# Kernel tuning notes

Hardware: AMD Instinct MI355X
Metric: run time of the kernel (lower is better)

The kernel has to match this reference:

```python
import jax, jax.numpy as jnp
import numpy as np

N_NODES = 100000
IN_DIM, HID_DIM, OUT_DIM = 1433, 16, 7
N_EDGES = 3200000


def gcn_conv(x, edge_index, W, b, num_nodes):
    # add self loops
    loop = jnp.arange(num_nodes, dtype=edge_index.dtype)
    src = jnp.concatenate([edge_index[0], loop])  # [E+N]
    dst = jnp.concatenate([edge_index[1], loop])
    h = x @ W + b  # [N, out]
    # degree computed on row (edge_index[0]) as in the torch code
    deg = jax.ops.segment_sum(jnp.ones_like(src, dtype=h.dtype), src,
                              num_segments=num_nodes)
    dis = deg ** -0.5  # self-loops guarantee deg >= 1
    norm = dis[src] * dis[dst]  # [E+N]
    msg = norm[:, None] * h[src]  # gather + scale
    return jax.ops.segment_sum(msg, dst, num_segments=num_nodes)  # scatter-add


def setup_inputs() -> dict:
    key = jax.random.key(0)
    k1, k2, k3, k4, k5, k6 = jax.random.split(key, 6)
    x = jax.random.normal(k1, (N_NODES, IN_DIM), dtype=jnp.float32)
    edge_index = jax.random.randint(k2, (2, N_EDGES), 0, N_NODES, dtype=jnp.int64)
    s1 = 1.0 / np.sqrt(IN_DIM)
    s2 = 1.0 / np.sqrt(HID_DIM)
    W1 = jax.random.uniform(k3, (IN_DIM, HID_DIM), jnp.float32, -s1, s1)
    b1 = jax.random.uniform(k4, (HID_DIM,), jnp.float32, -s1, s1)
    W2 = jax.random.uniform(k5, (HID_DIM, OUT_DIM), jnp.float32, -s2, s2)
    b2 = jax.random.uniform(k6, (OUT_DIM,), jnp.float32, -s2, s2)
    return {"x": x, "edge_index": edge_index, "W1": W1, "b1": b1,
            "W2": W2, "b2": b2}


def reference(x, edge_index, W1, b1, W2, b2):
    n = x.shape[0]
    h = gcn_conv(x, edge_index, W1, b1, n)
    h = jax.nn.relu(h)
    # dropout is inactive in eval mode (training=False)
    h = gcn_conv(h, edge_index, W2, b2, n)
    return jax.nn.log_softmax(h, axis=1)
```

## Files before the change

kernel.cpp:

```cpp
#include <hip/hip_runtime.h>
#include <math.h>

constexpr int IN_DIM = 1433;
constexpr int HID    = 16;
constexpr int OUTD   = 7;

__device__ __forceinline__ int edge_get(const int* __restrict__ ei, long long idx, int is64) {
    return is64 ? ei[2 * idx] : ei[idx];
}

__global__ void k_detect(const int* __restrict__ ei, int* __restrict__ flag) {
    __shared__ int nzsh;
    if (threadIdx.x == 0) nzsh = 0;
    __syncthreads();
    int nz = 0;
    for (int i = threadIdx.x; i < 2048; i += blockDim.x)
        nz |= (ei[2 * i + 1] != 0) ? 1 : 0;
    if (nz) nzsh = 1;
    __syncthreads();
    if (threadIdx.x == 0) *flag = (nzsh == 0) ? 1 : 0;
}

__global__ void k_init_new(int* __restrict__ deg, int* __restrict__ cnt, int n) {
    int i = blockIdx.x * blockDim.x + threadIdx.x;
    if (i < n) { deg[i] = 1; cnt[i] = 0; }
}

__global__ void k_deg_finish(float* __restrict__ dis, int n) {
    int i = blockIdx.x * blockDim.x + threadIdx.x;
    if (i < n) {
        int v = ((const int*)dis)[i];
        dis[i] = rsqrtf((float)v);
    }
}

__global__ __launch_bounds__(128) void k_gemm1h(
        const float* __restrict__ x, const float* __restrict__ W1,
        const float* __restrict__ b1, float* __restrict__ h1, int n,
        const int* __restrict__ ei, int E, const int* __restrict__ flag,
        int* __restrict__ deg, int* __restrict__ cnt, int nHist) {
    if ((int)blockIdx.x < nHist) {
        int is64 = *flag;
        long long stride = (long long)nHist * blockDim.x;
        for (long long e = (long long)blockIdx.x * blockDim.x + threadIdx.x;
             e < E; e += stride) {
            int s = edge_get(ei, e, is64);
            int d = edge_get(ei, (long long)E + e, is64);
            atomicAdd(&deg[s], 1);
            atomicAdd(&cnt[d], 1);
        }
        return;
    }

    constexpr int BK = 32, XST = 36;
    __shared__ __align__(16) float xs[128 * XST];
    __shared__ __align__(16) float wsm[BK * HID];
    const int t    = threadIdx.x;
    const int c4   = t & 3;
    const int rq   = t >> 2;
    const int row0 = ((int)blockIdx.x - nHist) * 128;

    float xreg[32];
    float wreg[4];
    float acc[16];
    #pragma unroll
    for (int j = 0; j < 16; ++j) acc[j] = 0.f;

    auto issue = [&](int kt) {
        #pragma unroll
        for (int i = 0; i < 32; ++i) {
            int idx  = t + 128 * i;
            int srow = idx >> 5;
            int scol = idx & 31;
            int gr   = row0 + srow;
            int col  = kt + scol;
            float v = 0.f;
            if (gr < n && col < IN_DIM) v = x[(long long)gr * IN_DIM + col];
            xreg[i] = v;
        }
        #pragma unroll
        for (int u = 0; u < 4; ++u) {
            int idx = t + 128 * u;
            int kk  = idx >> 4;
            wreg[u] = (kt + kk < IN_DIM) ? W1[(kt + kk) * HID + (idx & 15)] : 0.f;
        }
    };
    auto commit = [&]() {
        #pragma unroll
        for (int i = 0; i < 32; ++i) {
            int idx  = t + 128 * i;
            int srow = idx >> 5;
            int scol = idx & 31;
            xs[srow * XST + scol] = xreg[i];
        }
        #pragma unroll
        for (int u = 0; u < 4; ++u) wsm[t + 128 * u] = wreg[u];
    };

    const int nkt = (IN_DIM + BK - 1) / BK;
    issue(0);
    for (int it = 0; it < nkt; ++it) {
        commit();
        __syncthreads();
        if (it + 1 < nkt) issue((it + 1) * BK);
        #pragma unroll 8
        for (int k = 0; k < BK; ++k) {
            float4 w = *(const float4*)&wsm[k * HID + c4 * 4];
            #pragma unroll
            for (int j = 0; j < 4; ++j) {
                float xv = xs[(rq + 32 * j) * XST + k];
                acc[j * 4 + 0] += xv * w.x;
                acc[j * 4 + 1] += xv * w.y;
                acc[j * 4 + 2] += xv * w.z;
                acc[j * 4 + 3] += xv * w.w;
            }
        }
        __syncthreads();
    }

    float4 bv = *(const float4*)&b1[c4 * 4];
    #pragma unroll
    for (int j = 0; j < 4; ++j) {
        int gr = row0 + rq + 32 * j;
        if (gr < n) {
            float4 hv;
            hv.x = acc[j * 4 + 0] + bv.x;
            hv.y = acc[j * 4 + 1] + bv.y;
            hv.z = acc[j * 4 + 2] + bv.z;
            hv.w = acc[j * 4 + 3] + bv.w;
            *(float4*)&h1[(long long)gr * HID + c4 * 4] = hv;
        }
    }
}

__global__ void k_scale(const float* __restrict__ dis, const float* __restrict__ in,
                        float* __restrict__ out, int n, int squared) {
    int i = blockIdx.x * blockDim.x + threadIdx.x;
    if (i >= n * 4) return;
    int row = i >> 2;
    float d = dis[row];
    if (squared) d *= d;
    float4 v = *(const float4*)&in[(long long)i * 4];
    v.x *= d; v.y *= d; v.z *= d; v.w *= d;
    *(float4*)&out[(long long)i * 4] = v;
}

__global__ __launch_bounds__(256) void k_scan1(const int* __restrict__ cnt,
                                               int* __restrict__ bsum, int n) {
    __shared__ int sh[256];
    int t = threadIdx.x;
    int base = blockIdx.x * 1024 + t * 4;
    int s = 0;
    #pragma unroll
    for (int j = 0; j < 4; ++j) {
        int i = base + j;
        if (i < n) s += cnt[i];
    }
    sh[t] = s; __syncthreads();
    for (int o = 128; o > 0; o >>= 1) {
        if (t < o) sh[t] += sh[t + o];
        __syncthreads();
    }
    if (t == 0) bsum[blockIdx.x] = sh[0];
}

__global__ __launch_bounds__(256) void k_scan2(const int* __restrict__ bsum,
                                               int* __restrict__ boff,
                                               int* __restrict__ rp,
                                               int nb, int n, int E) {
    __shared__ int sh[256];
    int t = threadIdx.x;
    int v = (t < nb) ? bsum[t] : 0;
    sh[t] = v; __syncthreads();
    for (int o = 1; o < 256; o <<= 1) {
        int tmp = (t >= o) ? sh[t - o] : 0;
        __syncthreads();
        sh[t] += tmp;
        __syncthreads();
    }
    boff[t] = sh[t] - v;
    if (t == 0) rp[n] = E;
}

__global__ __launch_bounds__(256) void k_scan3(const int* __restrict__ cnt,
                                               const int* __restrict__ boff,
                                               int* __restrict__ rp,
                                               int* __restrict__ cur, int n) {
    __shared__ int sh[256];
    int t = threadIdx.x;
    int base = blockIdx.x * 1024 + t * 4;
    int c[4];
    int s = 0;
    #pragma unroll
    for (int j = 0; j < 4; ++j) {
        int i = base + j;
        c[j] = (i < n) ? cnt[i] : 0;
        s += c[j];
    }
    sh[t] = s; __syncthreads();
    for (int o = 1; o < 256; o <<= 1) {
        int tmp = (t >= o) ? sh[t - o] : 0;
        __syncthreads();
        sh[t] += tmp;
        __syncthreads();
    }
    int run = boff[blockIdx.x] + sh[t] - s;
    #pragma unroll
    for (int j = 0; j < 4; ++j) {
        int i = base + j;
        if (i < n) { rp[i] = run; cur[i] = run; }
        run += c[j];
    }
}

__global__ void k_fill(const int* __restrict__ ei, int E, const int* __restrict__ flag,
                       int* __restrict__ cur, int* __restrict__ csr) {
    int e = blockIdx.x * blockDim.x + threadIdx.x;
    if (e >= E) return;
    int is64 = *flag;
    int s = edge_get(ei, e, is64);
    int d = edge_get(ei, (long long)E + e, is64);
    int slot = atomicAdd(&cur[d], 1);
    csr[slot] = s;
}

__global__ __launch_bounds__(256) void k_gather1f(
        const int* __restrict__ rp, const int* __restrict__ csr,
        const float* __restrict__ dis, const float* __restrict__ hs1,
        const float* __restrict__ W2, const float* __restrict__ b2,
        float* __restrict__ hs2, int n) {
    __shared__ float w2s[HID * OUTD];
    __shared__ float b2s[OUTD];
    int t = threadIdx.x;
    if (t < HID * OUTD) w2s[t] = W2[t];
    if (t < OUTD) b2s[t] = b2[t];
    __syncthreads();

    int tid  = blockIdx.x * blockDim.x + t;
    int node = tid >> 2;
    int q    = tid & 3;
    if (node >= n) return;

    float4 acc = *(const float4*)&hs1[(long long)node * HID + q * 4];

    int i = rp[node], end = rp[node + 1];
    if (i < end) {
        int    s1  = csr[i];
        float4 hv1 = *(const float4*)&hs1[(long long)s1 * HID + q * 4];
        for (++i; i < end; ++i) {
            int    s2  = csr[i];
            float4 hv2 = *(const float4*)&hs1[(long long)s2 * HID + q * 4];
            acc.x += hv1.x; acc.y += hv1.y; acc.z += hv1.z; acc.w += hv1.w;
            hv1 = hv2;
        }
        acc.x += hv1.x; acc.y += hv1.y; acc.z += hv1.z; acc.w += hv1.w;
    }

    float dn = dis[node];
    float r0 = fmaxf(dn * acc.x, 0.f), r1 = fmaxf(dn * acc.y, 0.f);
    float r2 = fmaxf(dn * acc.z, 0.f), r3 = fmaxf(dn * acc.w, 0.f);
    float p[OUTD];
    #pragma unroll
    for (int j = 0; j < OUTD; ++j) {
        p[j] = r0 * w2s[(q * 4 + 0) * OUTD + j]
             + r1 * w2s[(q * 4 + 1) * OUTD + j]
             + r2 * w2s[(q * 4 + 2) * OUTD + j]
             + r3 * w2s[(q * 4 + 3) * OUTD + j];
    }
    #pragma unroll
    for (int j = 0; j < OUTD; ++j) {
        p[j] += __shfl_xor(p[j], 1, 4);
        p[j] += __shfl_xor(p[j], 2, 4);
    }
    hs2[(long long)node * OUTD + q] = dn * (p[q] + b2s[q]);
    if (q < 3) hs2[(long long)node * OUTD + q + 4] = dn * (p[q + 4] + b2s[q + 4]);
}

__global__ __launch_bounds__(256) void k_gather2(
        const int* __restrict__ rp, const int* __restrict__ csr,
        const float* __restrict__ dis, const float* __restrict__ hs2,
        float* __restrict__ out, int n) {
    int t = threadIdx.x;
    int node = blockIdx.x * 32 + (t >> 3);
    int q = t & 7;
    if (node >= n) return;
    float acc = -1e30f;
    if (q < OUTD) {
        acc = hs2[(long long)node * OUTD + q];
        int i = rp[node], end = rp[node + 1];
        if (i < end) {
            int   s1 = csr[i];
            float v1 = hs2[(long long)s1 * OUTD + q];
            for (++i; i < end; ++i) {
                int   s2 = csr[i];
                float v2 = hs2[(long long)s2 * OUTD + q];
                acc += v1;
                v1 = v2;
            }
            acc += v1;
        }
        acc *= dis[node];
    }
    float m = acc;
    #pragma unroll
    for (int o = 1; o < 8; o <<= 1) m = fmaxf(m, __shfl_xor(m, o, 8));
    float ex = (q < OUTD) ? expf(acc - m) : 0.f;
    float ss = ex;
    #pragma unroll
    for (int o = 1; o < 8; o <<= 1) ss += __shfl_xor(ss, o, 8);
    if (q < OUTD) out[(long long)node * OUTD + q] = acc - m - logf(ss);
}

__global__ void k_deg_init(int* __restrict__ deg, int n) {
    int i = blockIdx.x * blockDim.x + threadIdx.x;
    if (i < n) deg[i] = 1;
}

__global__ void k_deg_count(const int* __restrict__ ei, int E,
                            const int* __restrict__ flag, int* __restrict__ deg) {
    int e = blockIdx.x * blockDim.x + threadIdx.x;
    if (e >= E) return;
    int is64 = *flag;
    int s = edge_get(ei, e, is64);
    atomicAdd(&deg[s], 1);
}

__global__ void k_agg1(const int* __restrict__ ei, int E, const int* __restrict__ flag,
                       const float* __restrict__ dis, const float* __restrict__ h1,
                       float* __restrict__ a1) {
    long long tid = (long long)blockIdx.x * blockDim.x + threadIdx.x;
    int e = (int)(tid >> 2);
    int q = (int)(tid & 3);
    if (e >= E) return;
    int is64 = *flag;
    int s = edge_get(ei, e, is64);
    int d = edge_get(ei, (long long)E + e, is64);
    float nrm = dis[s] * dis[d];
    float4 v = *(const float4*)&h1[(long long)s * HID + q * 4];
    float* o = &a1[(long long)d * HID + q * 4];
    atomicAdd(o + 0, nrm * v.x);
    atomicAdd(o + 1, nrm * v.y);
    atomicAdd(o + 2, nrm * v.z);
    atomicAdd(o + 3, nrm * v.w);
}

__global__ __launch_bounds__(256) void k_gemm2(
        const float* __restrict__ a1, const float* __restrict__ W2,
        const float* __restrict__ b2, const float* __restrict__ dis,
        float* __restrict__ h2, float* __restrict__ a2, int n) {
    __shared__ float w2s[HID * OUTD];
    __shared__ float b2s[OUTD];
    int t = threadIdx.x;
    if (t < HID * OUTD) w2s[t] = W2[t];
    if (t < OUTD) b2s[t] = b2[t];
    __syncthreads();
    int r = blockIdx.x * blockDim.x + t;
    if (r >= n) return;
    float a[16];
    #pragma unroll
    for (int i = 0; i < 4; ++i) {
        float4 v = *(const float4*)&a1[(long long)r * HID + i * 4];
        a[4 * i + 0] = fmaxf(v.x, 0.f);
        a[4 * i + 1] = fmaxf(v.y, 0.f);
        a[4 * i + 2] = fmaxf(v.z, 0.f);
        a[4 * i + 3] = fmaxf(v.w, 0.f);
    }
    float dd = 0.f;
    if (a2) { float d = dis[r]; dd = d * d; }
    #pragma unroll
    for (int j = 0; j < OUTD; ++j) {
        float acc = b2s[j];
        #pragma unroll
        for (int k = 0; k < HID; ++k) acc += a[k] * w2s[k * OUTD + j];
        h2[(long long)r * OUTD + j] = acc;
        if (a2) a2[(long long)r * OUTD + j] = dd * acc;
    }
}

__global__ void k_agg2(const int* __restrict__ ei, int E, const int* __restrict__ flag,
                       const float* __restrict__ dis, const float* __restrict__ h2,
                       float* __restrict__ a2) {
    long long tid = (long long)blockIdx.x * blockDim.x + threadIdx.x;
    int e = (int)(tid >> 1);
    int q = (int)(tid & 1);
    if (e >= E) return;
    int is64 = *flag;
    int s = edge_get(ei, e, is64);
    int d = edge_get(ei, (long long)E + e, is64);
    float nrm = dis[s] * dis[d];
    int cnt = q ? 3 : 4;
    long long bs = (long long)s * OUTD + q * 4;
    long long bd = (long long)d * OUTD + q * 4;
    #pragma unroll
    for (int j = 0; j < 4; ++j)
        if (j < cnt) atomicAdd(&a2[bd + j], nrm * h2[bs + j]);
}

__global__ void k_lsm(const float* __restrict__ a2, float* __restrict__ out, int n) {
    int r = blockIdx.x * blockDim.x + threadIdx.x;
    if (r >= n) return;
    float v[OUTD];
    #pragma unroll
    for (int j = 0; j < OUTD; ++j) v[j] = a2[(long long)r * OUTD + j];
    float m = v[0];
    #pragma unroll
    for (int j = 1; j < OUTD; ++j) m = fmaxf(m, v[j]);
    float ssum = 0.f;
    #pragma unroll
    for (int j = 0; j < OUTD; ++j) ssum += expf(v[j] - m);
    float l = logf(ssum);
    #pragma unroll
    for (int j = 0; j < OUTD; ++j) out[(long long)r * OUTD + j] = v[j] - m - l;
}

extern "C" void kernel_launch(void* const* d_in, const int* in_sizes, int n_in,
                              void* d_out, int out_size, void* d_ws, size_t ws_size,
                              hipStream_t stream) {
    const float* x  = (const float*)d_in[0];
    const int*   ei = (const int*)d_in[1];
    const float* W1 = (const float*)d_in[2];
    const float* b1 = (const float*)d_in[3];
    const float* W2 = (const float*)d_in[4];
    const float* b2 = (const float*)d_in[5];
    float* out = (float*)d_out;

    const int N = in_sizes[0] / IN_DIM;
    const int E = in_sizes[1] / 2;

    const int TPB = 256;
    const int gN  = (N + TPB - 1) / TPB;
    const int gE  = (E + TPB - 1) / TPB;
    const int gG1 = (N + 127) / 128;
    const int NB  = (N + 1023) / 1024;
    const int nHist = 512;

    float* ws = (float*)d_ws;
    size_t o = 0;
    auto take = [&](size_t cnt) { size_t r = o; o += (cnt + 127) & ~(size_t)127; return r; };

    size_t off_dis  = take((size_t)N);
    size_t off_flag = take(64);
    size_t off_cnt  = take((size_t)N);
    size_t off_rp   = take((size_t)N + 1);
    size_t off_cur  = take((size_t)N);
    size_t off_bs   = take(256);
    size_t off_bo   = take(256);
    size_t off_csr  = take((size_t)E);
    size_t off_h1   = take((size_t)N * HID);
    size_t off_h2   = take((size_t)N * OUTD);
    size_t need_new = o * sizeof(float);

    if (ws_size >= need_new) {
        float* dis  = ws + off_dis;
        int*   degi = (int*)dis;
        int*   flag = (int*)(ws + off_flag);
        int*   cnt  = (int*)(ws + off_cnt);
        int*   rp   = (int*)(ws + off_rp);
        int*   cur  = (int*)(ws + off_cur);
        int*   bs   = (int*)(ws + off_bs);
        int*   bo   = (int*)(ws + off_bo);
        int*   csr  = (int*)(ws + off_csr);
        float* h1   = ws + off_h1;
        float* hs2  = ws + off_h2;

        k_detect<<<1, 256, 0, stream>>>(ei, flag);
        k_init_new<<<gN, TPB, 0, stream>>>(degi, cnt, N);
        k_gemm1h<<<nHist + gG1, 128, 0, stream>>>(x, W1, b1, h1, N,
                                                  ei, E, flag, degi, cnt, nHist);
        k_deg_finish<<<gN, TPB, 0, stream>>>(dis, N);
        k_scan1<<<NB, 256, 0, stream>>>(cnt, bs, N);
        k_scan2<<<1, 256, 0, stream>>>(bs, bo, rp, NB, N, E);
        k_scan3<<<NB, 256, 0, stream>>>(cnt, bo, rp, cur, N);
        k_scale<<<(int)(((long long)N * 4 + TPB - 1) / TPB), TPB, 0, stream>>>(
            dis, h1, h1, N, 0);
        k_fill<<<gE, TPB, 0, stream>>>(ei, E, flag, cur, csr);
        k_gather1f<<<(int)(((long long)N * 4 + TPB - 1) / TPB), TPB, 0, stream>>>(
            rp, csr, dis, h1, W2, b2, hs2, N);
        k_gather2<<<(N + 31) / 32, 256, 0, stream>>>(rp, csr, dis, hs2, out, N);
    } else {
        o = 0;
        size_t f_dis  = take((size_t)N);
        size_t f_flag = take(64);
        size_t f_h1   = take((size_t)N * HID);
        size_t f_a1   = take((size_t)N * HID);
        size_t f_h2   = take((size_t)N * OUTD);
        size_t f_a2   = take((size_t)N * OUTD);

        float* dis  = ws + f_dis;
        int*   degi = (int*)dis;
        int*   flag = (int*)(ws + f_flag);
        float* h1   = ws + f_h1;
        float* a1   = ws + f_a1;
        float* h2   = ws + f_h2;
        float* a2   = ws + f_a2;

        int g4E = (int)(((long long)4 * E + TPB - 1) / TPB);
        int g2E = (int)(((long long)2 * E + TPB - 1) / TPB);

        k_detect<<<1, 256, 0, stream>>>(ei, flag);
        k_deg_init<<<gN, TPB, 0, stream>>>(degi, N);
        k_deg_count<<<gE, TPB, 0, stream>>>(ei, E, flag, degi);
        k_deg_finish<<<gN, TPB, 0, stream>>>(dis, N);
        k_gemm1h<<<gG1, 128, 0, stream>>>(x, W1, b1, h1, N,
                                          ei, E, flag, nullptr, nullptr, 0);
        k_scale<<<(int)(((long long)N * 4 + TPB - 1) / TPB), TPB, 0, stream>>>(
            dis, h1, a1, N, 1);
        k_agg1<<<g4E, TPB, 0, stream>>>(ei, E, flag, dis, h1, a1);
        k_gemm2<<<gN, TPB, 0, stream>>>(a1, W2, b2, dis, h2, a2, N);
        k_agg2<<<g2E, TPB, 0, stream>>>(ei, E, flag, dis, h2, a2);
        k_lsm<<<gN, TPB, 0, stream>>>(a2, out, N);
    }
}
```

Measured before the change: 776.4 us.

## Replace shared-memory tiled first-layer GEMM with direct per-row float4 streaming

The first-layer GEMM no longer stages x and W1 tiles through LDS with register double-buffering. Each thread now streams its own x row with float4 loads, for two rows per thread, and reads W1 directly from global/cache. Block size goes from 128 to 256 threads, which also changes the work split of the fused histogram blocks. The aim is to drop LDS traffic and barriers in this memory-bound pass. The cost is strided, partly misaligned per-row global loads (row stride 1433), which may coalesce worse and lean on L1/L2 reuse.

Result: slower. 985.3 us (+26.9%).

```diff
diff --git a/kernel.cpp b/kernel.cpp
--- a/kernel.cpp
+++ b/kernel.cpp
@@ -34,7 +34,7 @@
     }
 }
 
-__global__ __launch_bounds__(128) void k_gemm1h(
+__global__ __launch_bounds__(256) void k_gemm1h(
         const float* __restrict__ x, const float* __restrict__ W1,
         const float* __restrict__ b1, float* __restrict__ h1, int n,
         const int* __restrict__ ei, int E, const int* __restrict__ flag,
@@ -52,84 +52,56 @@
         return;
     }
 
-    constexpr int BK = 32, XST = 36;
-    __shared__ __align__(16) float xs[128 * XST];
-    __shared__ __align__(16) float wsm[BK * HID];
     const int t    = threadIdx.x;
     const int c4   = t & 3;
-    const int rq   = t >> 2;
+    const int rr   = t >> 2;
     const int row0 = ((int)blockIdx.x - nHist) * 128;
-
-    float xreg[32];
-    float wreg[4];
-    float acc[16];
-    #pragma unroll
-    for (int j = 0; j < 16; ++j) acc[j] = 0.f;
-
-    auto issue = [&](int kt) {
-        #pragma unroll
-        for (int i = 0; i < 32; ++i) {
-            int idx  = t + 128 * i;
-            int srow = idx >> 5;
-            int scol = idx & 31;
-            int gr   = row0 + srow;
-            int col  = kt + scol;
-            float v = 0.f;
-            if (gr < n && col < IN_DIM) v = x[(long long)gr * IN_DIM + col];
-            xreg[i] = v;
-        }
-        #pragma unroll
-        for (int u = 0; u < 4; ++u) {
-            int idx = t + 128 * u;
-            int kk  = idx >> 4;
-            wreg[u] = (kt + kk < IN_DIM) ? W1[(kt + kk) * HID + (idx & 15)] : 0.f;
-        }
-    };
-    auto commit = [&]() {
-        #pragma unroll
-        for (int i = 0; i < 32; ++i) {
-            int idx  = t + 128 * i;
-            int srow = idx >> 5;
-            int scol = idx & 31;
-            xs[srow * XST + scol] = xreg[i];
-        }
-        #pragma unroll
-        for (int u = 0; u < 4; ++u) wsm[t + 128 * u] = wreg[u];
-    };
-
-    const int nkt = (IN_DIM + BK - 1) / BK;
-    issue(0);
-    for (int it = 0; it < nkt; ++it) {
-        commit();
-        __syncthreads();
-        if (it + 1 < nkt) issue((it + 1) * BK);
-        #pragma unroll 8
-        for (int k = 0; k < BK; ++k) {
-            float4 w = *(const float4*)&wsm[k * HID + c4 * 4];
-            #pragma unroll
-            for (int j = 0; j < 4; ++j) {
-                float xv = xs[(rq + 32 * j) * XST + k];
-                acc[j * 4 + 0] += xv * w.x;
-                acc[j * 4 + 1] += xv * w.y;
-                acc[j * 4 + 2] += xv * w.z;
-                acc[j * 4 + 3] += xv * w.w;
-            }
-        }
-        __syncthreads();
+    const int ra   = row0 + rr;
+    const int rb   = ra + 64;
+    const bool va  = ra < n;
+    const bool vb  = rb < n;
+    const float* pa = x + (long long)(va ? ra : (n - 1)) * IN_DIM;
+    const float* pb = x + (long long)(vb ? rb : (n - 1)) * IN_DIM;
+    const float* pw = W1 + c4 * 4;
+
+    float4 aa = make_float4(0.f, 0.f, 0.f, 0.f);
+    float4 ab = make_float4(0.f, 0.f, 0.f, 0.f);
+
+    int k = 0;
+    #pragma unroll 4
+    for (; k + 4 <= IN_DIM; k += 4) {
+        float4 xa = *(const float4*)(pa + k);
+        float4 xb = *(const float4*)(pb + k);
+        float4 w0 = *(const float4*)(pw + (long long)(k + 0) * HID);
+        float4 w1 = *(const float4*)(pw + (long long)(k + 1) * HID);
+        float4 w2 = *(const float4*)(pw + (long long)(k + 2) * HID);
+        float4 w3 = *(const float4*)(pw + (long long)(k + 3) * HID);
+        aa.x += xa.x * w0.x + xa.y * w1.x + xa.z * w2.x + xa.w * w3.x;
+        aa.y += xa.x * w0.y + xa.y * w1.y + xa.z * w2.y + xa.w * w3.y;
+        aa.z += xa.x * w0.z + xa.y * w1.z + xa.z * w2.z + xa.w * w3.z;
+        aa.w += xa.x * w0.w + xa.y * w1.w + xa.z * w2.w + xa.w * w3.w;
+        ab.x += xb.x * w0.x + xb.y * w1.x + xb.z * w2.x + xb.w * w3.x;
+        ab.y += xb.x * w0.y + xb.y * w1.y + xb.z * w2.y + xb.w * w3.y;
+        ab.z += xb.x * w0.z + xb.y * w1.z + xb.z * w2.z + xb.w * w3.z;
+        ab.w += xb.x * w0.w + xb.y * w1.w + xb.z * w2.w + xb.w * w3.w;
+    }
+    for (; k < IN_DIM; ++k) {
+        float4 w0 = *(const float4*)(pw + (long long)k * HID);
+        float xa = pa[k], xb = pb[k];
+        aa.x += xa * w0.x; aa.y += xa * w0.y; aa.z += xa * w0.z; aa.w += xa * w0.w;
+        ab.x += xb * w0.x; ab.y += xb * w0.y; ab.z += xb * w0.z; ab.w += xb * w0.w;
     }
 
     float4 bv = *(const float4*)&b1[c4 * 4];
-    #pragma unroll
-    for (int j = 0; j < 4; ++j) {
-        int gr = row0 + rq + 32 * j;
-        if (gr < n) {
-            float4 hv;
-            hv.x = acc[j * 4 + 0] + bv.x;
-            hv.y = acc[j * 4 + 1] + bv.y;
-            hv.z = acc[j * 4 + 2] + bv.z;
-            hv.w = acc[j * 4 + 3] + bv.w;
-            *(float4*)&h1[(long long)gr * HID + c4 * 4] = hv;
-        }
+    if (va) {
+        float4 hv;
+        hv.x = aa.x + bv.x; hv.y = aa.y + bv.y; hv.z = aa.z + bv.z; hv.w = aa.w + bv.w;
+        *(float4*)&h1[(long long)ra * HID + c4 * 4] = hv;
+    }
+    if (vb) {
+        float4 hv;
+        hv.x = ab.x + bv.x; hv.y = ab.y + bv.y; hv.z = ab.z + bv.z; hv.w = ab.w + bv.w;
+        *(float4*)&h1[(long long)rb * HID + c4 * 4] = hv;
     }
 }
 
@@ -465,7 +437,7 @@
 
         k_detect<<<1, 256, 0, stream>>>(ei, flag);
         k_init_new<<<gN, TPB, 0, stream>>>(degi, cnt, N);
-        k_gemm1h<<<nHist + gG1, 128, 0, stream>>>(x, W1, b1, h1, N,
+        k_gemm1h<<<nHist + gG1, 256, 0, stream>>>(x, W1, b1, h1, N,
                                                   ei, E, flag, degi, cnt, nHist);
         k_deg_finish<<<gN, TPB, 0, stream>>>(dis, N);
         k_scan1<<<NB, 256, 0, stream>>>(cnt, bs, N);
@@ -501,7 +473,7 @@
         k_deg_init<<<gN, TPB, 0, stream>>>(degi, N);
         k_deg_count<<<gE, TPB, 0, stream>>>(ei, E, flag, degi);
         k_deg_finish<<<gN, TPB, 0, stream>>>(dis, N);
-        k_gemm1h<<<gG1, 128, 0, stream>>>(x, W1, b1, h1, N,
+        k_gemm1h<<<gG1, 256, 0, stream>>>(x, W1, b1, h1, N,
                                           ei, E, flag, nullptr, nullptr, 0);
         k_scale<<<(int)(((long long)N * 4 + TPB - 1) / TPB), TPB, 0, stream>>>(
             dis, h1, a1, N, 1);
```
